# Performance work log

Hardware: AMD Instinct MI355X
Metric: run time of the kernel (lower is better)

## Reference

```python
import jax, jax.numpy as jnp
import numpy as np

B, T, H, W, C = 2, 4, 128, 128, 192
HEADS = 6
WS = 8          # attention window (per-frame, wsD=1)
OW = 12         # overlapping KV window: 8 + int(8*0.5)
PAD = (OW - WS) // 2
TBL = (WS + OW - 1) ** 2   # 361 relative-position-bias entries
MLP_HID = C * 2


def setup_inputs() -> dict:
    key = jax.random.key(0)
    ks = jax.random.split(key, 8)
    s = 0.02
    return dict(
        x=jax.random.normal(ks[0], (B, T, H, W, C), jnp.float32),
        x_size=jnp.array([H, W], jnp.int32),  # unused by forward (shadowed), kept for signature fidelity
        rpi_oca=jax.random.randint(ks[1], (WS * WS, OW * OW), 0, TBL),
        norm1_g=jnp.ones((C,), jnp.float32), norm1_b=jnp.zeros((C,), jnp.float32),
        qkv_w=jax.random.normal(ks[2], (C, 3 * C), jnp.float32) * s,
        qkv_b=jnp.zeros((3 * C,), jnp.float32),
        rpb_table=jax.random.normal(ks[3], (TBL, HEADS), jnp.float32) * s,
        norm2_g=jnp.ones((C,), jnp.float32), norm2_b=jnp.zeros((C,), jnp.float32),
        fc1_w=jax.random.normal(ks[4], (C, MLP_HID), jnp.float32) * s,
        fc1_b=jnp.zeros((MLP_HID,), jnp.float32),
        fc2_w=jax.random.normal(ks[5], (MLP_HID, C), jnp.float32) * s,
        fc2_b=jnp.zeros((C,), jnp.float32),
    )


def _ln(x, g, b):
    m = x.mean(-1, keepdims=True)
    v = ((x - m) ** 2).mean(-1, keepdims=True)
    return (x - m) * jax.lax.rsqrt(v + 1e-5) * g + b


def reference(x, x_size, rpi_oca, norm1_g, norm1_b, qkv_w, qkv_b, rpb_table,
              norm2_g, norm2_b, fc1_w, fc1_b, fc2_w, fc2_b):
    b, t, h, w, c = x.shape
    d = c // HEADS
    scale = d ** -0.5
    nH, nW = h // WS, w // WS
    b_ = b * t * nH * nW  # total windows
    shortcut = x
    xn = _ln(x, norm1_g, norm1_b)
    qkv = (xn @ qkv_w + qkv_b).reshape(b, t, h, w, 3, c)
    q, k, v = qkv[..., 0, :], qkv[..., 1, :], qkv[..., 2, :]
    # --- query: non-overlapping (1,8,8) windows -> (b_, heads, 64, d)
    qw = (q.reshape(b, t, nH, WS, nW, WS, c)
           .transpose(0, 1, 2, 4, 3, 5, 6)
           .reshape(b_, WS * WS, HEADS, d)
           .transpose(0, 2, 1, 3))
    # --- key/value: overlapping (1,12,12) windows with stride 8, zero-padded by 2
    hid = (jnp.arange(nH) * WS)[:, None] + jnp.arange(OW)  # (nH, OW)
    wid = (jnp.arange(nW) * WS)[:, None] + jnp.arange(OW)  # (nW, OW)

    def owin(z):
        zp = jnp.pad(z, ((0, 0), (0, 0), (PAD, PAD), (PAD, PAD), (0, 0)))
        zw = zp[:, :, hid][:, :, :, :, wid]  # (b, t, nH, OW, nW, OW, c)
        return (zw.transpose(0, 1, 2, 4, 3, 5, 6)
                  .reshape(b_, OW * OW, HEADS, d)
                  .transpose(0, 2, 1, 3))

    kw, vw = owin(k), owin(v)
    attn = jnp.einsum('bhqd,bhkd->bhqk', qw * scale, kw)  # (b_, heads, 64, 144)
    bias = rpb_table[rpi_oca.reshape(-1)].reshape(WS * WS, OW * OW, HEADS).transpose(2, 0, 1)
    attn = attn + bias[None]  # NOTE: original forward applies NO softmax (self.softmax unused)
    out = (jnp.einsum('bhqk,bhkd->bhqd', attn, vw)
             .transpose(0, 2, 1, 3)
             .reshape(b_, WS * WS, c))
    # window_reverse
    xa = (out.reshape(b, t, nH, nW, WS, WS, c)
             .transpose(0, 1, 2, 4, 3, 5, 6)
             .reshape(b, t, h, w, c))
    x = xa + shortcut  # self.proj is never applied in the original forward
    hmlp = jax.nn.gelu(_ln(x, norm2_g, norm2_b) @ fc1_w + fc1_b, approximate=False)
    return x + (hmlp @ fc2_w + fc2_b)
```

## Files before the change

### kernel.cpp

```cpp
#include <hip/hip_runtime.h>
#include <cstdint>
#include <cstddef>

typedef short bf16x8 __attribute__((ext_vector_type(8)));
typedef unsigned short u16x4 __attribute__((ext_vector_type(4)));
typedef float f32x4  __attribute__((ext_vector_type(4)));
typedef unsigned short u16;

#define DEVI __device__ __forceinline__

constexpr int C     = 192;
constexpr int HEADS = 6;
constexpr int NQKV  = 576;
constexpr int HID   = 384;
constexpr int NTOK  = 131072;

DEVI u16 f2bf(float f){
  union { float f; unsigned u; } v; v.f = f;
  return (u16)((v.u + 0x7fffu + ((v.u >> 16) & 1u)) >> 16);
}
DEVI float bf2f(u16 h){
  union { unsigned u; float f; } v; v.u = ((unsigned)h) << 16;
  return v.f;
}

DEVI float gelu(float xx){
  float y  = xx * 0.70710678118654752f;
  float ay = fabsf(y);
  float t  = __builtin_amdgcn_rcpf(1.0f + 0.3275911f * ay);
  float p  = t*(0.254829592f + t*(-0.284496736f + t*(1.421413741f + t*(-1.453152027f + t*1.061405429f))));
  float e  = __expf(-(y*y));
  float er = copysignf(1.0f - p*e, y);
  return 0.5f * xx * (1.0f + er);
}

__global__ void prep_kernel(const float* __restrict__ qkv_w,
                            const float* __restrict__ fc1_w,
                            const float* __restrict__ fc2_w,
                            const int*   __restrict__ rpi,
                            const float* __restrict__ rpb,
                            u16* __restrict__ qkvP,
                            u16* __restrict__ fc1P,
                            u16* __restrict__ fc2P,
                            float* __restrict__ bias_pk){
  int idx = blockIdx.x * blockDim.x + threadIdx.x;
  int stride = gridDim.x * blockDim.x;
  for(int i = idx; i < 36*6*64*8; i += stride){
    int e = i & 7, lane = (i >> 3) & 63, t = i >> 9;
    int ks = t % 6, p = t / 6;
    int n = p*16 + (lane & 15), k = ks*32 + (lane >> 4)*8 + e;
    qkvP[i] = f2bf(qkv_w[k*NQKV + n]);
  }
  for(int i = idx; i < 24*6*64*8; i += stride){
    int e = i & 7, lane = (i >> 3) & 63, t = i >> 9;
    int ks = t % 6, p = t / 6;
    int n = p*16 + (lane & 15), k = ks*32 + (lane >> 4)*8 + e;
    fc1P[i] = f2bf(fc1_w[k*HID + n]);
  }
  for(int i = idx; i < 12*12*64*8; i += stride){
    int e = i & 7, lane = (i >> 3) & 63, t = i >> 9;
    int ks = t % 12, p = t / 12;
    int n = p*16 + (lane & 15), k = ks*32 + (lane >> 4)*8 + e;
    fc2P[i] = f2bf(fc2_w[k*C + n]);
  }
  const int n4 = HEADS*5*2*4*64*4;
  for(int i = idx; i < n4; i += stride){
    int t = i;
    int r    = t & 3;  t >>= 2;
    int lane = t & 63; t >>= 6;
    int mi   = t & 3;  t >>= 2;
    int nf   = t & 1;  t >>= 1;
    int chunk = t % 5; int head = t / 5;
    int q  = mi*16 + (lane & 15);
    int kk = chunk*32 + nf*16 + ((lane >> 4) << 2) + r;
    float v = 0.f;
    if(kk < 144) v = rpb[rpi[q*144 + kk]*HEADS + head];
    bias_pk[i] = v;
  }
}

__global__ __launch_bounds__(384, 4)
void qkv_kernel(const float* __restrict__ x,
                const float* __restrict__ g1,
                const float* __restrict__ b1,
                const u16* __restrict__ wP,
                const float* __restrict__ qb,
                u16* __restrict__ qkv){
  __shared__ u16 xn[64][200];
  __shared__ u16 rp[64][152];
  const int tid = threadIdx.x;
  const int bid = blockIdx.x;
  const int nh = (bid >> 3) & 1;
  const int tb = (bid & 7) + ((bid >> 4) << 3);
  const size_t tok0 = (size_t)tb * 64;
  if(tid < 256){
    const int trow = tid >> 2;
    const int j = tid & 3;
    const float* xr = x + (tok0 + trow)*C;
    float4 xv[12];
    #pragma unroll
    for(int u = 0; u < 12; ++u)
      xv[u] = *reinterpret_cast<const float4*>(xr + u*16 + j*4);
    float s1 = 0.f, s2 = 0.f;
    #pragma unroll
    for(int u = 0; u < 12; ++u){
      const float* f = reinterpret_cast<const float*>(&xv[u]);
      #pragma unroll
      for(int e = 0; e < 4; ++e){ s1 += f[e]; s2 += f[e]*f[e]; }
    }
    s1 += __shfl_xor(s1, 1, 64); s2 += __shfl_xor(s2, 1, 64);
    s1 += __shfl_xor(s1, 2, 64); s2 += __shfl_xor(s2, 2, 64);
    const float mean = s1 * (1.f/192.f);
    const float rstd = rsqrtf(s2*(1.f/192.f) - mean*mean + 1e-5f);
    #pragma unroll
    for(int u = 0; u < 12; ++u){
      const float4 gv = *reinterpret_cast<const float4*>(g1 + u*16 + j*4);
      const float4 bv = *reinterpret_cast<const float4*>(b1 + u*16 + j*4);
      const float* f = reinterpret_cast<const float*>(&xv[u]);
      const float* gp = reinterpret_cast<const float*>(&gv);
      const float* bp = reinterpret_cast<const float*>(&bv);
      u16x4 pk;
      #pragma unroll
      for(int e = 0; e < 4; ++e) pk[e] = f2bf((f[e] - mean)*rstd*gp[e] + bp[e]);
      *reinterpret_cast<u16x4*>(&xn[trow][u*16 + j*4]) = pk;
    }
  }
  __syncthreads();
  const int lane = tid & 63;
  const int wn = tid >> 6;
  const int g = lane >> 4, col = lane & 15;
  const f32x4 fzero = {0.f, 0.f, 0.f, 0.f};
  f32x4 acc[4][3];
  #pragma unroll
  for(int mi = 0; mi < 4; ++mi)
    #pragma unroll
    for(int nf = 0; nf < 3; ++nf) acc[mi][nf] = fzero;
  const int p0 = nh*18 + wn*3;
  #pragma unroll
  for(int ks = 0; ks < 6; ++ks){
    bf16x8 wf[3];
    #pragma unroll
    for(int nf = 0; nf < 3; ++nf)
      wf[nf] = *reinterpret_cast<const bf16x8*>(wP + ((size_t)(((p0 + nf)*6 + ks)*64) + lane)*8);
    bf16x8 a[4];
    #pragma unroll
    for(int mi = 0; mi < 4; ++mi)
      a[mi] = *reinterpret_cast<const bf16x8*>(&xn[mi*16 + col][ks*32 + g*8]);
    #pragma unroll
    for(int nf = 0; nf < 3; ++nf)
      #pragma unroll
      for(int mi = 0; mi < 4; ++mi)
        acc[mi][nf] = __builtin_amdgcn_mfma_f32_16x16x32_bf16(a[mi], wf[nf], acc[mi][nf], 0, 0, 0);
  }
  #pragma unroll
  for(int ph = 0; ph < 2; ++ph){
    if(wn >= ph*3 && wn < ph*3 + 3){
      const int wl = wn - ph*3;
      #pragma unroll
      for(int mi = 0; mi < 4; ++mi){
        #pragma unroll
        for(int nf = 0; nf < 3; ++nf){
          const int nloc = wl*48 + nf*16 + col;
          const float bb = qb[nh*288 + ph*144 + nloc];
          #pragma unroll
          for(int r = 0; r < 4; ++r)
            rp[mi*16 + g*4 + r][nloc] = f2bf(acc[mi][nf][r] + bb);
        }
      }
    }
    __syncthreads();
    #pragma unroll
    for(int it = 0; it < 3; ++it){
      const int c = tid + it*384;
      const int tok = c / 18, cc = c - tok*18;
      const int n0 = nh*288 + ph*144 + cc*8;
      const int pl = n0 >> 5, d0 = n0 & 31;
      bf16x8 vv = *reinterpret_cast<const bf16x8*>(&rp[tok][cc*8]);
      *reinterpret_cast<bf16x8*>(qkv + ((size_t)pl*NTOK + tok0 + tok)*32 + d0) = vv;
    }
    __syncthreads();
  }
}

__global__ __launch_bounds__(256, 5)
void attn_kernel(const u16* __restrict__ qkv,
                 const float* __restrict__ bias_pk,
                 const float* __restrict__ x,
                 float* __restrict__ out){
  __shared__ alignas(16) char smem[28672];
  u16 (*Kl)[40]  = reinterpret_cast<u16(*)[40]>(smem);
  u16 (*Vt)[168] = reinterpret_cast<u16(*)[168]>(smem + 12800);
  char* Plb      = smem + 23552;
  float (*Of)[36] = reinterpret_cast<float(*)[36]>(smem);
  const int tid  = threadIdx.x;
  const int lane = tid & 63;
  const int w    = tid >> 6;
  const int g = lane >> 4, col = lane & 15;
  const int win = blockIdx.x, head = blockIdx.y;
  const int bt = win >> 8, wh = (win >> 4) & 15, ww = win & 15;
  const int h0 = wh*8, w0 = ww*8;
  const size_t tokbase = (size_t)bt * 16384;
  const u16* Qp = qkv + (size_t)head      *NTOK*32;
  const u16* Kp = qkv + (size_t)(6 + head)*NTOK*32;
  const u16* Vp = qkv + (size_t)(12 + head)*NTOK*32;
  const bf16x8 z8 = {0,0,0,0,0,0,0,0};

  #pragma unroll
  for(int ii = 0; ii < 3; ++ii){
    const int i = w + ii*4;
    if(i < 10){
      const int kr = i*16 + col;
      const int r12 = (kr*2731) >> 15;
      const int c12 = kr - r12*12;
      const int hh = h0 - 2 + r12;
      const int wp = w0 - 2 + c12;
      const bool valid = (kr < 144) && (hh >= 0) && (hh < 128) && (wp >= 0) && (wp < 128);
      const size_t t = valid ? (tokbase + (size_t)hh*128 + wp) : tokbase;
      bf16x8 kv_ = *reinterpret_cast<const bf16x8*>(Kp + t*32 + g*8);
      bf16x8 vv_ = *reinterpret_cast<const bf16x8*>(Vp + t*32 + g*8);
      kv_ = valid ? kv_ : z8;
      vv_ = valid ? vv_ : z8;
      *reinterpret_cast<bf16x8*>(&Kl[kr][g*8]) = kv_;
      #pragma unroll
      for(int e = 0; e < 8; ++e) Vt[g*8 + e][kr] = (u16)vv_[e];
    }
  }
  bf16x8 qf;
  {
    const int row = w*16 + col;
    const size_t t = tokbase + (size_t)(h0 + (row >> 3))*128 + (w0 + (row & 7));
    qf = *reinterpret_cast<const bf16x8*>(Qp + t*32 + g*8);
  }
  __syncthreads();

  const f32x4 fzero = {0.f, 0.f, 0.f, 0.f};
  f32x4 oacc[2];
  oacc[0] = fzero; oacc[1] = fzero;
  const float scale = 0.17677669529663689f;

  #pragma unroll
  for(int ch = 0; ch < 5; ++ch){
    float4 bv[2];
    #pragma unroll
    for(int nf = 0; nf < 2; ++nf)
      bv[nf] = *reinterpret_cast<const float4*>(
          bias_pk + (size_t)((((head*5 + ch)*2 + nf)*4 + w)*64 + lane)*4);
    bf16x8 kfr[2];
    #pragma unroll
    for(int nf = 0; nf < 2; ++nf)
      kfr[nf] = *reinterpret_cast<const bf16x8*>(&Kl[ch*32 + nf*16 + col][g*8]);
    f32x4 st[2];
    #pragma unroll
    for(int nf = 0; nf < 2; ++nf)
      st[nf] = __builtin_amdgcn_mfma_f32_16x16x32_bf16(kfr[nf], qf, fzero, 0, 0, 0);
    #pragma unroll
    for(int nf = 0; nf < 2; ++nf){
      const float* bp = reinterpret_cast<const float*>(&bv[nf]);
      const float p0 = fmaf(st[nf][0], scale, bp[0]);
      const float p1 = fmaf(st[nf][1], scale, bp[1]);
      const float p2 = fmaf(st[nf][2], scale, bp[2]);
      const float p3 = fmaf(st[nf][3], scale, bp[3]);
      uint2 pw;
      pw.x = (unsigned)f2bf(p0) | ((unsigned)f2bf(p1) << 16);
      pw.y = (unsigned)f2bf(p2) | ((unsigned)f2bf(p3) << 16);
      *reinterpret_cast<uint2*>(Plb + (w*16 + col)*80 + nf*32 + g*8) = pw;
    }
    bf16x8 pa = *reinterpret_cast<const bf16x8*>(Plb + (w*16 + col)*80 + g*16);
    bf16x8 vfr[2];
    #pragma unroll
    for(int nf = 0; nf < 2; ++nf)
      vfr[nf] = *reinterpret_cast<const bf16x8*>(&Vt[nf*16 + col][ch*32 + g*8]);
    #pragma unroll
    for(int nf = 0; nf < 2; ++nf)
      oacc[nf] = __builtin_amdgcn_mfma_f32_16x16x32_bf16(pa, vfr[nf], oacc[nf], 0, 0, 0);
  }
  __syncthreads();
  #pragma unroll
  for(int nf = 0; nf < 2; ++nf)
    #pragma unroll
    for(int r = 0; r < 4; ++r)
      Of[w*16 + g*4 + r][nf*16 + col] = oacc[nf][r];
  __syncthreads();
  {
    const int tok = tid >> 2, q = tid & 3;
    const int hh = h0 + (tok >> 3), wp = w0 + (tok & 7);
    const size_t o = (tokbase + (size_t)hh*128 + wp)*(size_t)C + head*32 + q*8;
    float4 a0 = *reinterpret_cast<const float4*>(&Of[tok][q*8]);
    float4 a1 = *reinterpret_cast<const float4*>(&Of[tok][q*8 + 4]);
    const float4 x0 = *reinterpret_cast<const float4*>(x + o);
    const float4 x1 = *reinterpret_cast<const float4*>(x + o + 4);
    a0.x += x0.x; a0.y += x0.y; a0.z += x0.z; a0.w += x0.w;
    a1.x += x1.x; a1.y += x1.y; a1.z += x1.z; a1.w += x1.w;
    *reinterpret_cast<float4*>(out + o)     = a0;
    *reinterpret_cast<float4*>(out + o + 4) = a1;
  }
}

__global__ __launch_bounds__(512, 6)
void mlp_kernel(float* __restrict__ io,
                const float* __restrict__ g2,
                const float* __restrict__ b2,
                const u16* __restrict__ w1P,
                const float* __restrict__ fb1,
                const u16* __restrict__ w2P,
                const float* __restrict__ fb2){
  __shared__ u16 xn[64][200];
  __shared__ u16 hq[64][136];
  const int tid = threadIdx.x;
  const size_t tok0 = (size_t)blockIdx.x * 64;
  {
    const int trow = tid >> 3;
    const int j = tid & 7;
    const float* xr = io + (tok0 + trow)*C;
    float4 xv[6];
    #pragma unroll
    for(int u = 0; u < 6; ++u)
      xv[u] = *reinterpret_cast<const float4*>(xr + u*32 + j*4);
    float s1 = 0.f, s2 = 0.f;
    #pragma unroll
    for(int u = 0; u < 6; ++u){
      const float* f = reinterpret_cast<const float*>(&xv[u]);
      #pragma unroll
      for(int e = 0; e < 4; ++e){ s1 += f[e]; s2 += f[e]*f[e]; }
    }
    s1 += __shfl_xor(s1, 1, 64); s2 += __shfl_xor(s2, 1, 64);
    s1 += __shfl_xor(s1, 2, 64); s2 += __shfl_xor(s2, 2, 64);
    s1 += __shfl_xor(s1, 4, 64); s2 += __shfl_xor(s2, 4, 64);
    const float mean = s1 * (1.f/192.f);
    const float rstd = rsqrtf(s2*(1.f/192.f) - mean*mean + 1e-5f);
    #pragma unroll
    for(int u = 0; u < 6; ++u){
      const float4 gv = *reinterpret_cast<const float4*>(g2 + u*32 + j*4);
      const float4 bv = *reinterpret_cast<const float4*>(b2 + u*32 + j*4);
      const float* f = reinterpret_cast<const float*>(&xv[u]);
      const float* gp = reinterpret_cast<const float*>(&gv);
      const float* bp = reinterpret_cast<const float*>(&bv);
      u16x4 pk;
      #pragma unroll
      for(int e = 0; e < 4; ++e) pk[e] = f2bf((f[e] - mean)*rstd*gp[e] + bp[e]);
      *reinterpret_cast<u16x4*>(&xn[trow][u*32 + j*4]) = pk;
    }
  }
  __syncthreads();
  const int lane = tid & 63, wave = tid >> 6;
  const int wm = wave >> 2;
  const int wn = wave & 3;
  const int g = lane >> 4, col = lane & 15;
  const f32x4 fzero = {0.f, 0.f, 0.f, 0.f};
  f32x4 acc2[2][3];
  #pragma unroll
  for(int mi = 0; mi < 2; ++mi)
    #pragma unroll
    for(int nf = 0; nf < 3; ++nf) acc2[mi][nf] = fzero;
  #pragma unroll
  for(int hb = 0; hb < 3; ++hb){
    f32x4 acc1[2][2];
    #pragma unroll
    for(int mi = 0; mi < 2; ++mi){ acc1[mi][0] = fzero; acc1[mi][1] = fzero; }
    #pragma unroll
    for(int ks = 0; ks < 6; ++ks){
      bf16x8 wf[2];
      #pragma unroll
      for(int nf = 0; nf < 2; ++nf){
        const int p = hb*8 + wn*2 + nf;
        wf[nf] = *reinterpret_cast<const bf16x8*>(w1P + ((size_t)((p*6 + ks)*64) + lane)*8);
      }
      bf16x8 a[2];
      #pragma unroll
      for(int mi = 0; mi < 2; ++mi)
        a[mi] = *reinterpret_cast<const bf16x8*>(&xn[wm*32 + mi*16 + col][ks*32 + g*8]);
      #pragma unroll
      for(int nf = 0; nf < 2; ++nf)
        #pragma unroll
        for(int mi = 0; mi < 2; ++mi)
          acc1[mi][nf] = __builtin_amdgcn_mfma_f32_16x16x32_bf16(a[mi], wf[nf], acc1[mi][nf], 0, 0, 0);
    }
    #pragma unroll
    for(int mi = 0; mi < 2; ++mi){
      #pragma unroll
      for(int nf = 0; nf < 2; ++nf){
        const int nl = wn*32 + nf*16 + col;
        const float bb = fb1[hb*128 + nl];
        #pragma unroll
        for(int r = 0; r < 4; ++r){
          const int row = wm*32 + mi*16 + g*4 + r;
          hq[row][nl] = f2bf(gelu(acc1[mi][nf][r] + bb));
        }
      }
    }
    __syncthreads();
    #pragma unroll
    for(int ks = 0; ks < 4; ++ks){
      const int ksg = hb*4 + ks;
      bf16x8 wf[3];
      #pragma unroll
      for(int nf = 0; nf < 3; ++nf)
        wf[nf] = *reinterpret_cast<const bf16x8*>(w2P + ((size_t)(((wn*3 + nf)*12 + ksg)*64) + lane)*8);
      bf16x8 a[2];
      #pragma unroll
      for(int mi = 0; mi < 2; ++mi)
        a[mi] = *reinterpret_cast<const bf16x8*>(&hq[wm*32 + mi*16 + col][ks*32 + g*8]);
      #pragma unroll
      for(int nf = 0; nf < 3; ++nf)
        #pragma unroll
        for(int mi = 0; mi < 2; ++mi)
          acc2[mi][nf] = __builtin_amdgcn_mfma_f32_16x16x32_bf16(a[mi], wf[nf], acc2[mi][nf], 0, 0, 0);
    }
    __syncthreads();
  }
  #pragma unroll
  for(int mi = 0; mi < 2; ++mi){
    #pragma unroll
    for(int nf = 0; nf < 3; ++nf){
      const int n = wn*48 + nf*16 + col;
      const float bb = fb2[n];
      #pragma unroll
      for(int r = 0; r < 4; ++r){
        const int row = wm*32 + mi*16 + g*4 + r;
        xn[row][n] = f2bf(acc2[mi][nf][r] + bb);
      }
    }
  }
  __syncthreads();
  {
    const int trow = tid >> 3, j = tid & 7;
    float* xr = io + (tok0 + trow)*C + j*24;
    #pragma unroll
    for(int u = 0; u < 6; ++u){
      const u16x4 s = *reinterpret_cast<const u16x4*>(&xn[trow][j*24 + u*4]);
      float4 v = *reinterpret_cast<const float4*>(xr + u*4);
      v.x += bf2f(s[0]); v.y += bf2f(s[1]); v.z += bf2f(s[2]); v.w += bf2f(s[3]);
      *reinterpret_cast<float4*>(xr + u*4) = v;
    }
  }
}

extern "C" void kernel_launch(void* const* d_in, const int* in_sizes, int n_in,
                              void* d_out, int out_size, void* d_ws, size_t ws_size,
                              hipStream_t stream){
  const float* x    = (const float*)d_in[0];
  const int*   rpi  = (const int*)  d_in[2];
  const float* n1g  = (const float*)d_in[3];
  const float* n1b  = (const float*)d_in[4];
  const float* qkvw = (const float*)d_in[5];
  const float* qkvb = (const float*)d_in[6];
  const float* rpb  = (const float*)d_in[7];
  const float* n2g  = (const float*)d_in[8];
  const float* n2b  = (const float*)d_in[9];
  const float* fc1w = (const float*)d_in[10];
  const float* fc1b = (const float*)d_in[11];
  const float* fc2w = (const float*)d_in[12];
  const float* fc2b = (const float*)d_in[13];
  float* out = (float*)d_out;
  char* ws = (char*)d_ws;
  u16*   qkvP    = (u16*)  (ws + 0);
  u16*   fc1P    = (u16*)  (ws + 221184);
  u16*   fc2P    = (u16*)  (ws + 368640);
  float* bias_pk = (float*)(ws + 516096);
  u16*   qkvbuf  = (u16*)  (ws + 1499136);
  if(ws_size < 152494080ull) return;
  prep_kernel<<<dim3(512), dim3(256), 0, stream>>>(qkvw, fc1w, fc2w, rpi, rpb, qkvP, fc1P, fc2P, bias_pk);
  qkv_kernel<<<dim3(4096), dim3(384), 0, stream>>>(x, n1g, n1b, qkvP, qkvb, qkvbuf);
  attn_kernel<<<dim3(2048, 6), dim3(256), 0, stream>>>(qkvbuf, bias_pk, x, out);
  mlp_kernel<<<dim3(2048), dim3(512), 0, stream>>>(out, n2g, n2b, fc1P, fc1b, fc2P, fc2b);
}
```

Measured before the change: 313.4 us.

## Restructure MLP kernel to six waves with full hidden tile in LDS

```diff
diff --git a/kernel.cpp b/kernel.cpp
--- a/kernel.cpp
+++ b/kernel.cpp
@@ -296,7 +296,7 @@
   }
 }
 
-__global__ __launch_bounds__(512, 6)
+__global__ __launch_bounds__(384, 3)
 void mlp_kernel(float* __restrict__ io,
                 const float* __restrict__ g2,
                 const float* __restrict__ b2,
@@ -305,132 +305,124 @@
                 const u16* __restrict__ w2P,
                 const float* __restrict__ fb2){
   __shared__ u16 xn[64][200];
-  __shared__ u16 hq[64][136];
+  __shared__ u16 hl[64][392];
   const int tid = threadIdx.x;
   const size_t tok0 = (size_t)blockIdx.x * 64;
-  {
-    const int trow = tid >> 3;
-    const int j = tid & 7;
+  if(tid < 256){
+    const int trow = tid >> 2;
+    const int j = tid & 3;
     const float* xr = io + (tok0 + trow)*C;
-    float4 xv[6];
-    #pragma unroll
-    for(int u = 0; u < 6; ++u)
-      xv[u] = *reinterpret_cast<const float4*>(xr + u*32 + j*4);
+    float4 xv[12];
+    #pragma unroll
+    for(int u = 0; u < 12; ++u)
+      xv[u] = *reinterpret_cast<const float4*>(xr + u*16 + j*4);
     float s1 = 0.f, s2 = 0.f;
     #pragma unroll
-    for(int u = 0; u < 6; ++u){
+    for(int u = 0; u < 12; ++u){
       const float* f = reinterpret_cast<const float*>(&xv[u]);
       #pragma unroll
       for(int e = 0; e < 4; ++e){ s1 += f[e]; s2 += f[e]*f[e]; }
     }
     s1 += __shfl_xor(s1, 1, 64); s2 += __shfl_xor(s2, 1, 64);
     s1 += __shfl_xor(s1, 2, 64); s2 += __shfl_xor(s2, 2, 64);
-    s1 += __shfl_xor(s1, 4, 64); s2 += __shfl_xor(s2, 4, 64);
     const float mean = s1 * (1.f/192.f);
     const float rstd = rsqrtf(s2*(1.f/192.f) - mean*mean + 1e-5f);
     #pragma unroll
-    for(int u = 0; u < 6; ++u){
-      const float4 gv = *reinterpret_cast<const float4*>(g2 + u*32 + j*4);
-      const float4 bv = *reinterpret_cast<const float4*>(b2 + u*32 + j*4);
+    for(int u = 0; u < 12; ++u){
+      const float4 gv = *reinterpret_cast<const float4*>(g2 + u*16 + j*4);
+      const float4 bv = *reinterpret_cast<const float4*>(b2 + u*16 + j*4);
       const float* f = reinterpret_cast<const float*>(&xv[u]);
       const float* gp = reinterpret_cast<const float*>(&gv);
       const float* bp = reinterpret_cast<const float*>(&bv);
       u16x4 pk;
       #pragma unroll
       for(int e = 0; e < 4; ++e) pk[e] = f2bf((f[e] - mean)*rstd*gp[e] + bp[e]);
-      *reinterpret_cast<u16x4*>(&xn[trow][u*32 + j*4]) = pk;
-    }
-  }
-  __syncthreads();
-  const int lane = tid & 63, wave = tid >> 6;
-  const int wm = wave >> 2;
-  const int wn = wave & 3;
+      *reinterpret_cast<u16x4*>(&xn[trow][u*16 + j*4]) = pk;
+    }
+  }
+  __syncthreads();
+  const int lane = tid & 63, w = tid >> 6;
   const int g = lane >> 4, col = lane & 15;
   const f32x4 fzero = {0.f, 0.f, 0.f, 0.f};
-  f32x4 acc2[2][3];
-  #pragma unroll
-  for(int mi = 0; mi < 2; ++mi)
-    #pragma unroll
-    for(int nf = 0; nf < 3; ++nf) acc2[mi][nf] = fzero;
-  #pragma unroll
-  for(int hb = 0; hb < 3; ++hb){
-    f32x4 acc1[2][2];
-    #pragma unroll
-    for(int mi = 0; mi < 2; ++mi){ acc1[mi][0] = fzero; acc1[mi][1] = fzero; }
-    #pragma unroll
-    for(int ks = 0; ks < 6; ++ks){
-      bf16x8 wf[2];
-      #pragma unroll
-      for(int nf = 0; nf < 2; ++nf){
-        const int p = hb*8 + wn*2 + nf;
-        wf[nf] = *reinterpret_cast<const bf16x8*>(w1P + ((size_t)((p*6 + ks)*64) + lane)*8);
+  f32x4 acc1[4][4];
+  #pragma unroll
+  for(int mi = 0; mi < 4; ++mi)
+    #pragma unroll
+    for(int nf = 0; nf < 4; ++nf) acc1[mi][nf] = fzero;
+  #pragma unroll
+  for(int ks = 0; ks < 6; ++ks){
+    bf16x8 wf[4];
+    #pragma unroll
+    for(int nf = 0; nf < 4; ++nf)
+      wf[nf] = *reinterpret_cast<const bf16x8*>(w1P + ((size_t)(((w*4 + nf)*6 + ks)*64) + lane)*8);
+    bf16x8 a[4];
+    #pragma unroll
+    for(int mi = 0; mi < 4; ++mi)
+      a[mi] = *reinterpret_cast<const bf16x8*>(&xn[mi*16 + col][ks*32 + g*8]);
+    #pragma unroll
+    for(int nf = 0; nf < 4; ++nf)
+      #pragma unroll
+      for(int mi = 0; mi < 4; ++mi)
+        acc1[mi][nf] = __builtin_amdgcn_mfma_f32_16x16x32_bf16(a[mi], wf[nf], acc1[mi][nf], 0, 0, 0);
+  }
+  #pragma unroll
+  for(int mi = 0; mi < 4; ++mi){
+    #pragma unroll
+    for(int nf = 0; nf < 4; ++nf){
+      const int nl = w*64 + nf*16 + col;
+      const float bb = fb1[nl];
+      #pragma unroll
+      for(int r = 0; r < 4; ++r){
+        const int row = mi*16 + g*4 + r;
+        hl[row][nl] = f2bf(gelu(acc1[mi][nf][r] + bb));
       }
-      bf16x8 a[2];
-      #pragma unroll
-      for(int mi = 0; mi < 2; ++mi)
-        a[mi] = *reinterpret_cast<const bf16x8*>(&xn[wm*32 + mi*16 + col][ks*32 + g*8]);
-      #pragma unroll
-      for(int nf = 0; nf < 2; ++nf)
-        #pragma unroll
-        for(int mi = 0; mi < 2; ++mi)
-          acc1[mi][nf] = __builtin_amdgcn_mfma_f32_16x16x32_bf16(a[mi], wf[nf], acc1[mi][nf], 0, 0, 0);
-    }
-    #pragma unroll
-    for(int mi = 0; mi < 2; ++mi){
-      #pragma unroll
-      for(int nf = 0; nf < 2; ++nf){
-        const int nl = wn*32 + nf*16 + col;
-        const float bb = fb1[hb*128 + nl];
-        #pragma unroll
-        for(int r = 0; r < 4; ++r){
-          const int row = wm*32 + mi*16 + g*4 + r;
-          hq[row][nl] = f2bf(gelu(acc1[mi][nf][r] + bb));
-        }
-      }
-    }
-    __syncthreads();
-    #pragma unroll
-    for(int ks = 0; ks < 4; ++ks){
-      const int ksg = hb*4 + ks;
-      bf16x8 wf[3];
-      #pragma unroll
-      for(int nf = 0; nf < 3; ++nf)
-        wf[nf] = *reinterpret_cast<const bf16x8*>(w2P + ((size_t)(((wn*3 + nf)*12 + ksg)*64) + lane)*8);
-      bf16x8 a[2];
-      #pragma unroll
-      for(int mi = 0; mi < 2; ++mi)
-        a[mi] = *reinterpret_cast<const bf16x8*>(&hq[wm*32 + mi*16 + col][ks*32 + g*8]);
-      #pragma unroll
-      for(int nf = 0; nf < 3; ++nf)
-        #pragma unroll
-        for(int mi = 0; mi < 2; ++mi)
-          acc2[mi][nf] = __builtin_amdgcn_mfma_f32_16x16x32_bf16(a[mi], wf[nf], acc2[mi][nf], 0, 0, 0);
-    }
-    __syncthreads();
-  }
-  #pragma unroll
-  for(int mi = 0; mi < 2; ++mi){
-    #pragma unroll
-    for(int nf = 0; nf < 3; ++nf){
-      const int n = wn*48 + nf*16 + col;
+    }
+  }
+  __syncthreads();
+  f32x4 acc2[4][2];
+  #pragma unroll
+  for(int mi = 0; mi < 4; ++mi){ acc2[mi][0] = fzero; acc2[mi][1] = fzero; }
+  #pragma unroll
+  for(int ks = 0; ks < 12; ++ks){
+    bf16x8 wf[2];
+    #pragma unroll
+    for(int nf = 0; nf < 2; ++nf)
+      wf[nf] = *reinterpret_cast<const bf16x8*>(w2P + ((size_t)(((w*2 + nf)*12 + ks)*64) + lane)*8);
+    bf16x8 a[4];
+    #pragma unroll
+    for(int mi = 0; mi < 4; ++mi)
+      a[mi] = *reinterpret_cast<const bf16x8*>(&hl[mi*16 + col][ks*32 + g*8]);
+    #pragma unroll
+    for(int nf = 0; nf < 2; ++nf)
+      #pragma unroll
+      for(int mi = 0; mi < 4; ++mi)
+        acc2[mi][nf] = __builtin_amdgcn_mfma_f32_16x16x32_bf16(a[mi], wf[nf], acc2[mi][nf], 0, 0, 0);
+  }
+  #pragma unroll
+  for(int mi = 0; mi < 4; ++mi){
+    #pragma unroll
+    for(int nf = 0; nf < 2; ++nf){
+      const int n = w*32 + nf*16 + col;
       const float bb = fb2[n];
       #pragma unroll
       for(int r = 0; r < 4; ++r){
-        const int row = wm*32 + mi*16 + g*4 + r;
+        const int row = mi*16 + g*4 + r;
         xn[row][n] = f2bf(acc2[mi][nf][r] + bb);
       }
     }
   }
   __syncthreads();
   {
-    const int trow = tid >> 3, j = tid & 7;
-    float* xr = io + (tok0 + trow)*C + j*24;
-    #pragma unroll
-    for(int u = 0; u < 6; ++u){
-      const u16x4 s = *reinterpret_cast<const u16x4*>(&xn[trow][j*24 + u*4]);
-      float4 v = *reinterpret_cast<const float4*>(xr + u*4);
-      v.x += bf2f(s[0]); v.y += bf2f(s[1]); v.z += bf2f(s[2]); v.w += bf2f(s[3]);
-      *reinterpret_cast<float4*>(xr + u*4) = v;
+    const int trow = tid / 6, j = tid - trow*6;
+    if(trow < 64){
+      float* xr = io + (tok0 + trow)*C + j*32;
+      #pragma unroll
+      for(int u = 0; u < 8; ++u){
+        const u16x4 s = *reinterpret_cast<const u16x4*>(&xn[trow][j*32 + u*4]);
+        float4 v = *reinterpret_cast<const float4*>(xr + u*4);
+        v.x += bf2f(s[0]); v.y += bf2f(s[1]); v.z += bf2f(s[2]); v.w += bf2f(s[3]);
+        *reinterpret_cast<float4*>(xr + u*4) = v;
+      }
     }
   }
 }
@@ -462,5 +454,5 @@
   prep_kernel<<<dim3(512), dim3(256), 0, stream>>>(qkvw, fc1w, fc2w, rpi, rpb, qkvP, fc1P, fc2P, bias_pk);
   qkv_kernel<<<dim3(4096), dim3(384), 0, stream>>>(x, n1g, n1b, qkvP, qkvb, qkvbuf);
   attn_kernel<<<dim3(2048, 6), dim3(256), 0, stream>>>(qkvbuf, bias_pk, x, out);
-  mlp_kernel<<<dim3(2048), dim3(512), 0, stream>>>(out, n2g, n2b, fc1P, fc1b, fc2P, fc2b);
-}
+  mlp_kernel<<<dim3(2048), dim3(384), 0, stream>>>(out, n2g, n2b, fc1P, fc1b, fc2P, fc2b);
+}
```

After: 328.7 us. 1.05x slower.

## Batch attention K/V/bias loads up front and double-buffer MLP weight fragments

Applied to the files above, without the earlier changes.

```diff
diff --git a/kernel.cpp b/kernel.cpp
--- a/kernel.cpp
+++ b/kernel.cpp
@@ -182,7 +182,7 @@
   }
 }
 
-__global__ __launch_bounds__(256, 5)
+__global__ __launch_bounds__(256, 4)
 void attn_kernel(const u16* __restrict__ qkv,
                  const float* __restrict__ bias_pk,
                  const float* __restrict__ x,
@@ -205,32 +205,54 @@
   const u16* Vp = qkv + (size_t)(12 + head)*NTOK*32;
   const bf16x8 z8 = {0,0,0,0,0,0,0,0};
 
+  int   gi[3];  gi[0] = w;  gi[1] = w + 4;  gi[2] = (w + 8 > 9) ? 9 : (w + 8);
+  size_t ta[3]; bool tv[3]; int krr[3];
   #pragma unroll
   for(int ii = 0; ii < 3; ++ii){
-    const int i = w + ii*4;
-    if(i < 10){
-      const int kr = i*16 + col;
-      const int r12 = (kr*2731) >> 15;
-      const int c12 = kr - r12*12;
-      const int hh = h0 - 2 + r12;
-      const int wp = w0 - 2 + c12;
-      const bool valid = (kr < 144) && (hh >= 0) && (hh < 128) && (wp >= 0) && (wp < 128);
-      const size_t t = valid ? (tokbase + (size_t)hh*128 + wp) : tokbase;
-      bf16x8 kv_ = *reinterpret_cast<const bf16x8*>(Kp + t*32 + g*8);
-      bf16x8 vv_ = *reinterpret_cast<const bf16x8*>(Vp + t*32 + g*8);
-      kv_ = valid ? kv_ : z8;
-      vv_ = valid ? vv_ : z8;
-      *reinterpret_cast<bf16x8*>(&Kl[kr][g*8]) = kv_;
-      #pragma unroll
-      for(int e = 0; e < 8; ++e) Vt[g*8 + e][kr] = (u16)vv_[e];
-    }
-  }
+    const int kr = gi[ii]*16 + col;
+    const int r12 = (kr*2731) >> 15;
+    const int c12 = kr - r12*12;
+    const int hh = h0 - 2 + r12;
+    const int wp = w0 - 2 + c12;
+    tv[ii] = (kr < 144) && (hh >= 0) && (hh < 128) && (wp >= 0) && (wp < 128);
+    ta[ii] = tv[ii] ? (tokbase + (size_t)hh*128 + wp) : tokbase;
+    krr[ii] = kr;
+  }
+  bf16x8 k0 = *reinterpret_cast<const bf16x8*>(Kp + ta[0]*32 + g*8);
+  bf16x8 v0 = *reinterpret_cast<const bf16x8*>(Vp + ta[0]*32 + g*8);
+  bf16x8 k1 = *reinterpret_cast<const bf16x8*>(Kp + ta[1]*32 + g*8);
+  bf16x8 v1 = *reinterpret_cast<const bf16x8*>(Vp + ta[1]*32 + g*8);
+  bf16x8 k2 = *reinterpret_cast<const bf16x8*>(Kp + ta[2]*32 + g*8);
+  bf16x8 v2 = *reinterpret_cast<const bf16x8*>(Vp + ta[2]*32 + g*8);
   bf16x8 qf;
   {
     const int row = w*16 + col;
     const size_t t = tokbase + (size_t)(h0 + (row >> 3))*128 + (w0 + (row & 7));
     qf = *reinterpret_cast<const bf16x8*>(Qp + t*32 + g*8);
   }
+  asm volatile("" : "+v"(k0), "+v"(v0), "+v"(k1), "+v"(v1), "+v"(k2), "+v"(v2), "+v"(qf));
+  k0 = tv[0] ? k0 : z8;  v0 = tv[0] ? v0 : z8;
+  k1 = tv[1] ? k1 : z8;  v1 = tv[1] ? v1 : z8;
+  k2 = tv[2] ? k2 : z8;  v2 = tv[2] ? v2 : z8;
+  *reinterpret_cast<bf16x8*>(&Kl[krr[0]][g*8]) = k0;
+  *reinterpret_cast<bf16x8*>(&Kl[krr[1]][g*8]) = k1;
+  *reinterpret_cast<bf16x8*>(&Kl[krr[2]][g*8]) = k2;
+  #pragma unroll
+  for(int e = 0; e < 8; ++e){
+    Vt[g*8 + e][krr[0]] = (u16)v0[e];
+    Vt[g*8 + e][krr[1]] = (u16)v1[e];
+    Vt[g*8 + e][krr[2]] = (u16)v2[e];
+  }
+  f32x4 bv[5][2];
+  #pragma unroll
+  for(int ch = 0; ch < 5; ++ch)
+    #pragma unroll
+    for(int nf = 0; nf < 2; ++nf)
+      bv[ch][nf] = *reinterpret_cast<const f32x4*>(
+          bias_pk + (size_t)((((head*5 + ch)*2 + nf)*4 + w)*64 + lane)*4);
+  asm volatile("" : "+v"(bv[0][0]), "+v"(bv[0][1]), "+v"(bv[1][0]), "+v"(bv[1][1]),
+                    "+v"(bv[2][0]), "+v"(bv[2][1]), "+v"(bv[3][0]), "+v"(bv[3][1]),
+                    "+v"(bv[4][0]), "+v"(bv[4][1]));
   __syncthreads();
 
   const f32x4 fzero = {0.f, 0.f, 0.f, 0.f};
@@ -240,11 +262,6 @@
 
   #pragma unroll
   for(int ch = 0; ch < 5; ++ch){
-    float4 bv[2];
-    #pragma unroll
-    for(int nf = 0; nf < 2; ++nf)
-      bv[nf] = *reinterpret_cast<const float4*>(
-          bias_pk + (size_t)((((head*5 + ch)*2 + nf)*4 + w)*64 + lane)*4);
     bf16x8 kfr[2];
     #pragma unroll
     for(int nf = 0; nf < 2; ++nf)
@@ -255,11 +272,10 @@
       st[nf] = __builtin_amdgcn_mfma_f32_16x16x32_bf16(kfr[nf], qf, fzero, 0, 0, 0);
     #pragma unroll
     for(int nf = 0; nf < 2; ++nf){
-      const float* bp = reinterpret_cast<const float*>(&bv[nf]);
-      const float p0 = fmaf(st[nf][0], scale, bp[0]);
-      const float p1 = fmaf(st[nf][1], scale, bp[1]);
-      const float p2 = fmaf(st[nf][2], scale, bp[2]);
-      const float p3 = fmaf(st[nf][3], scale, bp[3]);
+      const float p0 = fmaf(st[nf][0], scale, bv[ch][nf][0]);
+      const float p1 = fmaf(st[nf][1], scale, bv[ch][nf][1]);
+      const float p2 = fmaf(st[nf][2], scale, bv[ch][nf][2]);
+      const float p3 = fmaf(st[nf][3], scale, bv[ch][nf][3]);
       uint2 pw;
       pw.x = (unsigned)f2bf(p0) | ((unsigned)f2bf(p1) << 16);
       pw.y = (unsigned)f2bf(p2) | ((unsigned)f2bf(p3) << 16);
@@ -296,7 +312,7 @@
   }
 }
 
-__global__ __launch_bounds__(512, 6)
+__global__ __launch_bounds__(512, 4)
 void mlp_kernel(float* __restrict__ io,
                 const float* __restrict__ g2,
                 const float* __restrict__ b2,
@@ -305,7 +321,7 @@
                 const u16* __restrict__ w2P,
                 const float* __restrict__ fb2){
   __shared__ u16 xn[64][200];
-  __shared__ u16 hq[64][136];
+  __shared__ u16 hl[64][200];
   const int tid = threadIdx.x;
   const size_t tok0 = (size_t)blockIdx.x * 64;
   {
@@ -353,58 +369,71 @@
     #pragma unroll
     for(int nf = 0; nf < 3; ++nf) acc2[mi][nf] = fzero;
   #pragma unroll
-  for(int hb = 0; hb < 3; ++hb){
-    f32x4 acc1[2][2];
-    #pragma unroll
-    for(int mi = 0; mi < 2; ++mi){ acc1[mi][0] = fzero; acc1[mi][1] = fzero; }
+  for(int hb = 0; hb < 2; ++hb){
+    f32x4 acc1[2][3];
+    #pragma unroll
+    for(int mi = 0; mi < 2; ++mi)
+      #pragma unroll
+      for(int nf = 0; nf < 3; ++nf) acc1[mi][nf] = fzero;
+    bf16x8 wf0 = *reinterpret_cast<const bf16x8*>(w1P + ((size_t)(((hb*12 + wn*3 + 0)*6 + 0)*64) + lane)*8);
+    bf16x8 wf1 = *reinterpret_cast<const bf16x8*>(w1P + ((size_t)(((hb*12 + wn*3 + 1)*6 + 0)*64) + lane)*8);
+    bf16x8 wf2 = *reinterpret_cast<const bf16x8*>(w1P + ((size_t)(((hb*12 + wn*3 + 2)*6 + 0)*64) + lane)*8);
     #pragma unroll
     for(int ks = 0; ks < 6; ++ks){
-      bf16x8 wf[2];
-      #pragma unroll
-      for(int nf = 0; nf < 2; ++nf){
-        const int p = hb*8 + wn*2 + nf;
-        wf[nf] = *reinterpret_cast<const bf16x8*>(w1P + ((size_t)((p*6 + ks)*64) + lane)*8);
+      bf16x8 wn0, wn1, wn2;
+      if(ks < 5){
+        wn0 = *reinterpret_cast<const bf16x8*>(w1P + ((size_t)(((hb*12 + wn*3 + 0)*6 + ks+1)*64) + lane)*8);
+        wn1 = *reinterpret_cast<const bf16x8*>(w1P + ((size_t)(((hb*12 + wn*3 + 1)*6 + ks+1)*64) + lane)*8);
+        wn2 = *reinterpret_cast<const bf16x8*>(w1P + ((size_t)(((hb*12 + wn*3 + 2)*6 + ks+1)*64) + lane)*8);
       }
       bf16x8 a[2];
       #pragma unroll
       for(int mi = 0; mi < 2; ++mi)
         a[mi] = *reinterpret_cast<const bf16x8*>(&xn[wm*32 + mi*16 + col][ks*32 + g*8]);
       #pragma unroll
-      for(int nf = 0; nf < 2; ++nf)
-        #pragma unroll
-        for(int mi = 0; mi < 2; ++mi)
-          acc1[mi][nf] = __builtin_amdgcn_mfma_f32_16x16x32_bf16(a[mi], wf[nf], acc1[mi][nf], 0, 0, 0);
+      for(int mi = 0; mi < 2; ++mi){
+        acc1[mi][0] = __builtin_amdgcn_mfma_f32_16x16x32_bf16(a[mi], wf0, acc1[mi][0], 0, 0, 0);
+        acc1[mi][1] = __builtin_amdgcn_mfma_f32_16x16x32_bf16(a[mi], wf1, acc1[mi][1], 0, 0, 0);
+        acc1[mi][2] = __builtin_amdgcn_mfma_f32_16x16x32_bf16(a[mi], wf2, acc1[mi][2], 0, 0, 0);
+      }
+      if(ks < 5){ wf0 = wn0; wf1 = wn1; wf2 = wn2; }
     }
     #pragma unroll
     for(int mi = 0; mi < 2; ++mi){
       #pragma unroll
-      for(int nf = 0; nf < 2; ++nf){
-        const int nl = wn*32 + nf*16 + col;
-        const float bb = fb1[hb*128 + nl];
+      for(int nf = 0; nf < 3; ++nf){
+        const int nl = wn*48 + nf*16 + col;
+        const float bb = fb1[hb*192 + nl];
         #pragma unroll
         for(int r = 0; r < 4; ++r){
           const int row = wm*32 + mi*16 + g*4 + r;
-          hq[row][nl] = f2bf(gelu(acc1[mi][nf][r] + bb));
+          hl[row][nl] = f2bf(gelu(acc1[mi][nf][r] + bb));
         }
       }
     }
     __syncthreads();
-    #pragma unroll
-    for(int ks = 0; ks < 4; ++ks){
-      const int ksg = hb*4 + ks;
-      bf16x8 wf[3];
-      #pragma unroll
-      for(int nf = 0; nf < 3; ++nf)
-        wf[nf] = *reinterpret_cast<const bf16x8*>(w2P + ((size_t)(((wn*3 + nf)*12 + ksg)*64) + lane)*8);
+    bf16x8 uf0 = *reinterpret_cast<const bf16x8*>(w2P + ((size_t)(((wn*3 + 0)*12 + hb*6 + 0)*64) + lane)*8);
+    bf16x8 uf1 = *reinterpret_cast<const bf16x8*>(w2P + ((size_t)(((wn*3 + 1)*12 + hb*6 + 0)*64) + lane)*8);
+    bf16x8 uf2 = *reinterpret_cast<const bf16x8*>(w2P + ((size_t)(((wn*3 + 2)*12 + hb*6 + 0)*64) + lane)*8);
+    #pragma unroll
+    for(int ks = 0; ks < 6; ++ks){
+      bf16x8 un0, un1, un2;
+      if(ks < 5){
+        un0 = *reinterpret_cast<const bf16x8*>(w2P + ((size_t)(((wn*3 + 0)*12 + hb*6 + ks+1)*64) + lane)*8);
+        un1 = *reinterpret_cast<const bf16x8*>(w2P + ((size_t)(((wn*3 + 1)*12 + hb*6 + ks+1)*64) + lane)*8);
+        un2 = *reinterpret_cast<const bf16x8*>(w2P + ((size_t)(((wn*3 + 2)*12 + hb*6 + ks+1)*64) + lane)*8);
+      }
       bf16x8 a[2];
       #pragma unroll
       for(int mi = 0; mi < 2; ++mi)
-        a[mi] = *reinterpret_cast<const bf16x8*>(&hq[wm*32 + mi*16 + col][ks*32 + g*8]);
-      #pragma unroll
-      for(int nf = 0; nf < 3; ++nf)
-        #pragma unroll
-        for(int mi = 0; mi < 2; ++mi)
-          acc2[mi][nf] = __builtin_amdgcn_mfma_f32_16x16x32_bf16(a[mi], wf[nf], acc2[mi][nf], 0, 0, 0);
+        a[mi] = *reinterpret_cast<const bf16x8*>(&hl[wm*32 + mi*16 + col][ks*32 + g*8]);
+      #pragma unroll
+      for(int mi = 0; mi < 2; ++mi){
+        acc2[mi][0] = __builtin_amdgcn_mfma_f32_16x16x32_bf16(a[mi], uf0, acc2[mi][0], 0, 0, 0);
+        acc2[mi][1] = __builtin_amdgcn_mfma_f32_16x16x32_bf16(a[mi], uf1, acc2[mi][1], 0, 0, 0);
+        acc2[mi][2] = __builtin_amdgcn_mfma_f32_16x16x32_bf16(a[mi], uf2, acc2[mi][2], 0, 0, 0);
+      }
+      if(ks < 5){ uf0 = un0; uf1 = un1; uf2 = un2; }
     }
     __syncthreads();
   }
```

New measurement: 292.4 us. -6.7%, faster.

## Store attention residual as bf16 and widen MLP hidden tiles

Applied to the files above, without the earlier changes.

```diff
diff --git a/kernel.cpp b/kernel.cpp
--- a/kernel.cpp
+++ b/kernel.cpp
@@ -182,11 +182,13 @@
   }
 }
 
+template<bool X1B>
 __global__ __launch_bounds__(256, 5)
 void attn_kernel(const u16* __restrict__ qkv,
                  const float* __restrict__ bias_pk,
                  const float* __restrict__ x,
-                 float* __restrict__ out){
+                 float* __restrict__ out,
+                 u16* __restrict__ x1b){
   __shared__ alignas(16) char smem[28672];
   u16 (*Kl)[40]  = reinterpret_cast<u16(*)[40]>(smem);
   u16 (*Vt)[168] = reinterpret_cast<u16(*)[168]>(smem + 12800);
@@ -284,20 +286,32 @@
   {
     const int tok = tid >> 2, q = tid & 3;
     const int hh = h0 + (tok >> 3), wp = w0 + (tok & 7);
-    const size_t o = (tokbase + (size_t)hh*128 + wp)*(size_t)C + head*32 + q*8;
+    const size_t trow = tokbase + (size_t)hh*128 + wp;
+    const size_t o = trow*(size_t)C + head*32 + q*8;
     float4 a0 = *reinterpret_cast<const float4*>(&Of[tok][q*8]);
     float4 a1 = *reinterpret_cast<const float4*>(&Of[tok][q*8 + 4]);
     const float4 x0 = *reinterpret_cast<const float4*>(x + o);
     const float4 x1 = *reinterpret_cast<const float4*>(x + o + 4);
     a0.x += x0.x; a0.y += x0.y; a0.z += x0.z; a0.w += x0.w;
     a1.x += x1.x; a1.y += x1.y; a1.z += x1.z; a1.w += x1.w;
-    *reinterpret_cast<float4*>(out + o)     = a0;
-    *reinterpret_cast<float4*>(out + o + 4) = a1;
-  }
-}
-
-__global__ __launch_bounds__(512, 6)
+    if(X1B){
+      bf16x8 pk;
+      pk[0] = (short)f2bf(a0.x); pk[1] = (short)f2bf(a0.y);
+      pk[2] = (short)f2bf(a0.z); pk[3] = (short)f2bf(a0.w);
+      pk[4] = (short)f2bf(a1.x); pk[5] = (short)f2bf(a1.y);
+      pk[6] = (short)f2bf(a1.z); pk[7] = (short)f2bf(a1.w);
+      *reinterpret_cast<bf16x8*>(x1b + o) = pk;
+    }else{
+      *reinterpret_cast<float4*>(out + o)     = a0;
+      *reinterpret_cast<float4*>(out + o + 4) = a1;
+    }
+  }
+}
+
+template<bool X1B>
+__global__ __launch_bounds__(512, 4)
 void mlp_kernel(float* __restrict__ io,
+                const u16* __restrict__ x1b,
                 const float* __restrict__ g2,
                 const float* __restrict__ b2,
                 const u16* __restrict__ w1P,
@@ -305,40 +319,60 @@
                 const u16* __restrict__ w2P,
                 const float* __restrict__ fb2){
   __shared__ u16 xn[64][200];
-  __shared__ u16 hq[64][136];
+  __shared__ u16 hl[64][200];
   const int tid = threadIdx.x;
   const size_t tok0 = (size_t)blockIdx.x * 64;
   {
     const int trow = tid >> 3;
     const int j = tid & 7;
-    const float* xr = io + (tok0 + trow)*C;
-    float4 xv[6];
-    #pragma unroll
-    for(int u = 0; u < 6; ++u)
-      xv[u] = *reinterpret_cast<const float4*>(xr + u*32 + j*4);
+    float v[24];
+    if(X1B){
+      const u16* xr = x1b + (tok0 + trow)*C + j*24;
+      bf16x8 b0 = *reinterpret_cast<const bf16x8*>(xr);
+      bf16x8 b1 = *reinterpret_cast<const bf16x8*>(xr + 8);
+      bf16x8 b2_ = *reinterpret_cast<const bf16x8*>(xr + 16);
+      #pragma unroll
+      for(int e = 0; e < 8; ++e){ v[e] = bf2f((u16)b0[e]); v[8+e] = bf2f((u16)b1[e]); v[16+e] = bf2f((u16)b2_[e]); }
+    }else{
+      const float* xr = io + (tok0 + trow)*C;
+      #pragma unroll
+      for(int u = 0; u < 6; ++u){
+        const float4 t = *reinterpret_cast<const float4*>(xr + u*32 + j*4);
+        v[u*4+0] = t.x; v[u*4+1] = t.y; v[u*4+2] = t.z; v[u*4+3] = t.w;
+      }
+    }
     float s1 = 0.f, s2 = 0.f;
     #pragma unroll
-    for(int u = 0; u < 6; ++u){
-      const float* f = reinterpret_cast<const float*>(&xv[u]);
-      #pragma unroll
-      for(int e = 0; e < 4; ++e){ s1 += f[e]; s2 += f[e]*f[e]; }
-    }
+    for(int e = 0; e < 24; ++e){ s1 += v[e]; s2 += v[e]*v[e]; }
     s1 += __shfl_xor(s1, 1, 64); s2 += __shfl_xor(s2, 1, 64);
     s1 += __shfl_xor(s1, 2, 64); s2 += __shfl_xor(s2, 2, 64);
     s1 += __shfl_xor(s1, 4, 64); s2 += __shfl_xor(s2, 4, 64);
     const float mean = s1 * (1.f/192.f);
     const float rstd = rsqrtf(s2*(1.f/192.f) - mean*mean + 1e-5f);
-    #pragma unroll
-    for(int u = 0; u < 6; ++u){
-      const float4 gv = *reinterpret_cast<const float4*>(g2 + u*32 + j*4);
-      const float4 bv = *reinterpret_cast<const float4*>(b2 + u*32 + j*4);
-      const float* f = reinterpret_cast<const float*>(&xv[u]);
-      const float* gp = reinterpret_cast<const float*>(&gv);
-      const float* bp = reinterpret_cast<const float*>(&bv);
-      u16x4 pk;
-      #pragma unroll
-      for(int e = 0; e < 4; ++e) pk[e] = f2bf((f[e] - mean)*rstd*gp[e] + bp[e]);
-      *reinterpret_cast<u16x4*>(&xn[trow][u*32 + j*4]) = pk;
+    if(X1B){
+      #pragma unroll
+      for(int u = 0; u < 6; ++u){
+        const float4 gv = *reinterpret_cast<const float4*>(g2 + j*24 + u*4);
+        const float4 bv = *reinterpret_cast<const float4*>(b2 + j*24 + u*4);
+        const float* gp = reinterpret_cast<const float*>(&gv);
+        const float* bp = reinterpret_cast<const float*>(&bv);
+        u16x4 pk;
+        #pragma unroll
+        for(int e = 0; e < 4; ++e) pk[e] = f2bf((v[u*4+e] - mean)*rstd*gp[e] + bp[e]);
+        *reinterpret_cast<u16x4*>(&xn[trow][j*24 + u*4]) = pk;
+      }
+    }else{
+      #pragma unroll
+      for(int u = 0; u < 6; ++u){
+        const float4 gv = *reinterpret_cast<const float4*>(g2 + u*32 + j*4);
+        const float4 bv = *reinterpret_cast<const float4*>(b2 + u*32 + j*4);
+        const float* gp = reinterpret_cast<const float*>(&gv);
+        const float* bp = reinterpret_cast<const float*>(&bv);
+        u16x4 pk;
+        #pragma unroll
+        for(int e = 0; e < 4; ++e) pk[e] = f2bf((v[u*4+e] - mean)*rstd*gp[e] + bp[e]);
+        *reinterpret_cast<u16x4*>(&xn[trow][u*32 + j*4]) = pk;
+      }
     }
   }
   __syncthreads();
@@ -353,24 +387,24 @@
     #pragma unroll
     for(int nf = 0; nf < 3; ++nf) acc2[mi][nf] = fzero;
   #pragma unroll
-  for(int hb = 0; hb < 3; ++hb){
-    f32x4 acc1[2][2];
-    #pragma unroll
-    for(int mi = 0; mi < 2; ++mi){ acc1[mi][0] = fzero; acc1[mi][1] = fzero; }
+  for(int hb = 0; hb < 2; ++hb){
+    f32x4 acc1[2][3];
+    #pragma unroll
+    for(int mi = 0; mi < 2; ++mi)
+      #pragma unroll
+      for(int nf = 0; nf < 3; ++nf) acc1[mi][nf] = fzero;
     #pragma unroll
     for(int ks = 0; ks < 6; ++ks){
-      bf16x8 wf[2];
-      #pragma unroll
-      for(int nf = 0; nf < 2; ++nf){
-        const int p = hb*8 + wn*2 + nf;
-        wf[nf] = *reinterpret_cast<const bf16x8*>(w1P + ((size_t)((p*6 + ks)*64) + lane)*8);
-      }
+      bf16x8 wf[3];
+      #pragma unroll
+      for(int nf = 0; nf < 3; ++nf)
+        wf[nf] = *reinterpret_cast<const bf16x8*>(w1P + ((size_t)(((hb*12 + wn*3 + nf)*6 + ks)*64) + lane)*8);
       bf16x8 a[2];
       #pragma unroll
       for(int mi = 0; mi < 2; ++mi)
         a[mi] = *reinterpret_cast<const bf16x8*>(&xn[wm*32 + mi*16 + col][ks*32 + g*8]);
       #pragma unroll
-      for(int nf = 0; nf < 2; ++nf)
+      for(int nf = 0; nf < 3; ++nf)
         #pragma unroll
         for(int mi = 0; mi < 2; ++mi)
           acc1[mi][nf] = __builtin_amdgcn_mfma_f32_16x16x32_bf16(a[mi], wf[nf], acc1[mi][nf], 0, 0, 0);
@@ -378,28 +412,27 @@
     #pragma unroll
     for(int mi = 0; mi < 2; ++mi){
       #pragma unroll
-      for(int nf = 0; nf < 2; ++nf){
-        const int nl = wn*32 + nf*16 + col;
-        const float bb = fb1[hb*128 + nl];
+      for(int nf = 0; nf < 3; ++nf){
+        const int nl = wn*48 + nf*16 + col;
+        const float bb = fb1[hb*192 + nl];
         #pragma unroll
         for(int r = 0; r < 4; ++r){
           const int row = wm*32 + mi*16 + g*4 + r;
-          hq[row][nl] = f2bf(gelu(acc1[mi][nf][r] + bb));
+          hl[row][nl] = f2bf(gelu(acc1[mi][nf][r] + bb));
         }
       }
     }
     __syncthreads();
     #pragma unroll
-    for(int ks = 0; ks < 4; ++ks){
-      const int ksg = hb*4 + ks;
+    for(int ks = 0; ks < 6; ++ks){
       bf16x8 wf[3];
       #pragma unroll
       for(int nf = 0; nf < 3; ++nf)
-        wf[nf] = *reinterpret_cast<const bf16x8*>(w2P + ((size_t)(((wn*3 + nf)*12 + ksg)*64) + lane)*8);
+        wf[nf] = *reinterpret_cast<const bf16x8*>(w2P + ((size_t)(((wn*3 + nf)*12 + hb*6 + ks)*64) + lane)*8);
       bf16x8 a[2];
       #pragma unroll
       for(int mi = 0; mi < 2; ++mi)
-        a[mi] = *reinterpret_cast<const bf16x8*>(&hq[wm*32 + mi*16 + col][ks*32 + g*8]);
+        a[mi] = *reinterpret_cast<const bf16x8*>(&hl[wm*32 + mi*16 + col][ks*32 + g*8]);
       #pragma unroll
       for(int nf = 0; nf < 3; ++nf)
         #pragma unroll
@@ -408,29 +441,56 @@
     }
     __syncthreads();
   }
-  #pragma unroll
-  for(int mi = 0; mi < 2; ++mi){
-    #pragma unroll
-    for(int nf = 0; nf < 3; ++nf){
-      const int n = wn*48 + nf*16 + col;
-      const float bb = fb2[n];
-      #pragma unroll
-      for(int r = 0; r < 4; ++r){
-        const int row = wm*32 + mi*16 + g*4 + r;
-        xn[row][n] = f2bf(acc2[mi][nf][r] + bb);
-      }
-    }
-  }
-  __syncthreads();
-  {
+  if(X1B){
+    #pragma unroll
+    for(int mi = 0; mi < 2; ++mi){
+      #pragma unroll
+      for(int nf = 0; nf < 3; ++nf){
+        const int n = wn*48 + nf*16 + col;
+        const float bb = fb2[n];
+        #pragma unroll
+        for(int r = 0; r < 4; ++r){
+          const int row = wm*32 + mi*16 + g*4 + r;
+          xn[row][n] = f2bf(acc2[mi][nf][r] + bb);
+        }
+      }
+    }
+    __syncthreads();
     const int trow = tid >> 3, j = tid & 7;
-    float* xr = io + (tok0 + trow)*C + j*24;
+    const u16* xq = x1b + (tok0 + trow)*C + j*24;
+    float* op = io + (tok0 + trow)*C + j*24;
+    bf16x8 r0 = *reinterpret_cast<const bf16x8*>(xq);
+    bf16x8 r1 = *reinterpret_cast<const bf16x8*>(xq + 8);
+    bf16x8 r2 = *reinterpret_cast<const bf16x8*>(xq + 16);
+    bf16x8 m0 = *reinterpret_cast<const bf16x8*>(&xn[trow][j*24]);
+    bf16x8 m1 = *reinterpret_cast<const bf16x8*>(&xn[trow][j*24 + 8]);
+    bf16x8 m2 = *reinterpret_cast<const bf16x8*>(&xn[trow][j*24 + 16]);
+    float ov[24];
+    #pragma unroll
+    for(int e = 0; e < 8; ++e){
+      ov[e]    = bf2f((u16)r0[e]) + bf2f((u16)m0[e]);
+      ov[8+e]  = bf2f((u16)r1[e]) + bf2f((u16)m1[e]);
+      ov[16+e] = bf2f((u16)r2[e]) + bf2f((u16)m2[e]);
+    }
     #pragma unroll
     for(int u = 0; u < 6; ++u){
-      const u16x4 s = *reinterpret_cast<const u16x4*>(&xn[trow][j*24 + u*4]);
-      float4 v = *reinterpret_cast<const float4*>(xr + u*4);
-      v.x += bf2f(s[0]); v.y += bf2f(s[1]); v.z += bf2f(s[2]); v.w += bf2f(s[3]);
-      *reinterpret_cast<float4*>(xr + u*4) = v;
+      float4 t; t.x = ov[u*4]; t.y = ov[u*4+1]; t.z = ov[u*4+2]; t.w = ov[u*4+3];
+      *reinterpret_cast<float4*>(op + u*4) = t;
+    }
+  }else{
+    #pragma unroll
+    for(int mi = 0; mi < 2; ++mi){
+      #pragma unroll
+      for(int nf = 0; nf < 3; ++nf){
+        const int n = wn*48 + nf*16 + col;
+        const float bb = fb2[n];
+        #pragma unroll
+        for(int r = 0; r < 4; ++r){
+          const int row = wm*32 + mi*16 + g*4 + r;
+          const size_t idx = (tok0 + row)*C + n;
+          io[idx] = acc2[mi][nf][r] + bb + io[idx];
+        }
+      }
     }
   }
 }
@@ -458,9 +518,16 @@
   u16*   fc2P    = (u16*)  (ws + 368640);
   float* bias_pk = (float*)(ws + 516096);
   u16*   qkvbuf  = (u16*)  (ws + 1499136);
+  u16*   x1b     = (u16*)  (ws + 152494080);
   if(ws_size < 152494080ull) return;
+  const bool big = ws_size >= 202825728ull;
   prep_kernel<<<dim3(512), dim3(256), 0, stream>>>(qkvw, fc1w, fc2w, rpi, rpb, qkvP, fc1P, fc2P, bias_pk);
   qkv_kernel<<<dim3(4096), dim3(384), 0, stream>>>(x, n1g, n1b, qkvP, qkvb, qkvbuf);
-  attn_kernel<<<dim3(2048, 6), dim3(256), 0, stream>>>(qkvbuf, bias_pk, x, out);
-  mlp_kernel<<<dim3(2048), dim3(512), 0, stream>>>(out, n2g, n2b, fc1P, fc1b, fc2P, fc2b);
-}
+  if(big){
+    attn_kernel<true><<<dim3(2048, 6), dim3(256), 0, stream>>>(qkvbuf, bias_pk, x, out, x1b);
+    mlp_kernel<true><<<dim3(2048), dim3(512), 0, stream>>>(out, x1b, n2g, n2b, fc1P, fc1b, fc2P, fc2b);
+  }else{
+    attn_kernel<false><<<dim3(2048, 6), dim3(256), 0, stream>>>(qkvbuf, bias_pk, x, out, nullptr);
+    mlp_kernel<false><<<dim3(2048), dim3(512), 0, stream>>>(out, nullptr, n2g, n2b, fc1P, fc1b, fc2P, fc2b);
+  }
+}
```

Measured after the change: 284.0 us. 1.1x faster.
